# Optimization experiments

Hardware: AMD Instinct MI355X
Metric: run time of the kernel (lower is better)

The kernel has to match this reference:

```python
import jax, jax.numpy as jnp
import numpy as np

NUM_HEADS = 8  # matches init_kwargs num_heads
LN_EPS = 1e-5  # torch.nn.LayerNorm default


def setup_inputs() -> dict:
    key = jax.random.key(0)
    ks = jax.random.split(key, 12)
    E, B, H, S = 16384, 16, 256, 32
    edge_features = jax.random.normal(ks[0], (E, H), jnp.float32)
    edge_coords = jax.random.normal(ks[1], (E, 3), jnp.float32)
    # sorted, equal-size segments (all graphs non-empty)
    batch = jnp.repeat(jnp.arange(B, dtype=jnp.int32), E // B)
    s_h = 1.0 / np.sqrt(H)
    s_sh = 1.0 / np.sqrt(S * H)
    seed_vectors = jax.random.normal(ks[2], (S, H), jnp.float32)
    # weights stored [in, out] (transposed vs torch nn.Linear)
    Wq = jax.random.normal(ks[3], (H, H), jnp.float32) * s_h
    Wk = jax.random.normal(ks[4], (H, H), jnp.float32) * s_h
    Wv = jax.random.normal(ks[5], (H, H), jnp.float32) * s_h
    Wo = jax.random.normal(ks[6], (H, H), jnp.float32) * s_h
    bo = jnp.zeros((H,), jnp.float32)
    ln_g = jnp.ones((H,), jnp.float32)
    ln_b = jnp.zeros((H,), jnp.float32)
    W1 = jax.random.normal(ks[7], (S * H, H), jnp.float32) * s_sh
    b1 = jnp.zeros((H,), jnp.float32)
    W2 = jax.random.normal(ks[8], (H, H), jnp.float32) * s_h
    b2 = jnp.zeros((H,), jnp.float32)
    return dict(edge_features=edge_features, edge_coords=edge_coords, batch=batch,
                seed_vectors=seed_vectors, Wq=Wq, Wk=Wk, Wv=Wv, Wo=Wo, bo=bo,
                ln_g=ln_g, ln_b=ln_b, W1=W1, b1=b1, W2=W2, b2=b2, num_graphs=B)


def reference(edge_features, edge_coords, batch, seed_vectors, Wq, Wk, Wv, Wo, bo,
              ln_g, ln_b, W1, b1, W2, b2, num_graphs):
    S, H = seed_vectors.shape
    nh = NUM_HEADS
    hd = H // nh
    q = (seed_vectors @ Wq).reshape(S, nh, hd)          # shared across graphs
    k = (edge_features @ Wk).reshape(-1, nh, hd)        # [E, nh, hd]
    v = (edge_features @ Wv).reshape(-1, nh, hd)
    scores = jnp.einsum('shd,ehd->esh', q, k) / np.sqrt(hd).astype(np.float32)
    # segment softmax over edges within each graph
    m = jax.lax.stop_gradient(jax.ops.segment_max(scores, batch, num_segments=num_graphs))
    num = jnp.exp(scores - m[batch])
    den = jax.ops.segment_sum(num, batch, num_segments=num_graphs)
    w = num / den[batch]                                # [E, S, nh]
    att = jax.ops.segment_sum(jnp.einsum('esh,ehd->eshd', w, v), batch,
                              num_segments=num_graphs)  # [B, S, nh, hd]
    att = att.reshape(num_graphs, S, H)                 # concat heads (head-major)
    y = seed_vectors[None, :, :] + att @ Wo + bo        # residual + out_proj
    mu = jnp.mean(y, axis=-1, keepdims=True)
    var = jnp.mean((y - mu) ** 2, axis=-1, keepdims=True)
    y = (y - mu) / jnp.sqrt(var + LN_EPS) * ln_g + ln_b
    flat = y.reshape(num_graphs, S * H)
    h1 = jax.nn.silu(flat @ W1 + b1)
    return h1 @ W2 + b2                                 # [B, H]
```

## Files before the change

### kernel.cpp

```cpp
#include <hip/hip_runtime.h>
#include <math.h>
#include <stdint.h>

#define E_EDGES 16384
#define H_DIM   256
#define S_SEEDS 32
#define NHEADS  8
#define HDIM    32
#define BGRAPHS 16
#define EPG     1024
#define NCHUNK  256
#define CPG     16
#define RSQRT_HD 0.17677669529663687f

typedef __attribute__((ext_vector_type(8))) short bf16x8;
typedef __attribute__((ext_vector_type(4))) float f32x4;

__device__ inline unsigned short f2bf(float x) {
    unsigned u = __float_as_uint(x);
    u += 0x7fff + ((u >> 16) & 1);
    return (unsigned short)(u >> 16);
}
__device__ inline float bf2f(unsigned int h) {
    return __uint_as_float((h & 0xffffu) << 16);
}
__device__ inline unsigned pack2(float a, float b) {
    return (unsigned)f2bf(a) | ((unsigned)f2bf(b) << 16);
}

__global__ __launch_bounds__(256) void k_wc(const float* __restrict__ Wv,
                                            const float* __restrict__ Wk,
                                            const float* __restrict__ Wq,
                                            const float* __restrict__ seed,
                                            unsigned short* __restrict__ WcT) {
    int j = blockIdx.x;
    int i = threadIdx.x;
    float val;
    if (j < H_DIM) {
        val = Wv[i * H_DIM + j];
    } else {
        int c = j - H_DIM;
        int h = c >> 5, s = c & 31;
        __shared__ float qp[8][33];
        __shared__ float qrow[HDIM];
        int d = i & 31, g = i >> 5;
        const float* wq = &Wq[(g * 32) * H_DIM + h * HDIM + d];
        const float* sd = &seed[s * H_DIM + g * 32];
        float p = 0.f;
        #pragma unroll
        for (int ii = 0; ii < 32; ++ii)
            p = fmaf(sd[ii], wq[(size_t)ii * H_DIM], p);
        qp[g][d] = p;
        __syncthreads();
        if (i < HDIM) {
            float qv = 0.f;
            #pragma unroll
            for (int g2 = 0; g2 < 8; ++g2) qv += qp[g2][i];
            qrow[i] = qv;
        }
        __syncthreads();
        const float* wk = &Wk[i * H_DIM + h * HDIM];
        float acc = 0.f;
        #pragma unroll
        for (int dd = 0; dd < HDIM; dd += 4) {
            float4 w = *(const float4*)&wk[dd];
            float4 qq = *(const float4*)&qrow[dd];
            acc = fmaf(w.x, qq.x, acc); acc = fmaf(w.y, qq.y, acc);
            acc = fmaf(w.z, qq.z, acc); acc = fmaf(w.w, qq.w, acc);
        }
        val = acc * RSQRT_HD;
    }
    WcT[j * H_DIM + i] = f2bf(val);
}

struct SMattn {
    unsigned short As[64][264];
    unsigned short Vt[256][72];
    unsigned short Pt[256][72];
};

__global__ __launch_bounds__(512) void k_attn(const float* __restrict__ A,
                                              const unsigned short* __restrict__ WcT,
                                              float* __restrict__ outc,
                                              float* __restrict__ mg,
                                              float* __restrict__ sg) {
    __shared__ SMattn sm;
    int tid = threadIdx.x;
    int chunk = blockIdx.x;
    int e0 = chunk * 64;
    int w = tid >> 6, lane = tid & 63;
    int lr = lane & 15, kg = lane >> 4;

    {
        int r = tid >> 3, cg8 = tid & 7;
        const float* ap = &A[(size_t)(e0 + r) * H_DIM + cg8 * 32];
        #pragma unroll
        for (int i = 0; i < 4; ++i) {
            float4 x = *(const float4*)&ap[i * 8];
            float4 y = *(const float4*)&ap[i * 8 + 4];
            uint4 o;
            o.x = pack2(x.x, x.y); o.y = pack2(x.z, x.w);
            o.z = pack2(y.x, y.y); o.w = pack2(y.z, y.w);
            *(uint4*)&sm.As[r][cg8 * 32 + i * 8] = o;
        }
    }
    __syncthreads();

    const unsigned short* brow = &WcT[(size_t)(w * 64 + lr) * H_DIM + kg * 8];
    uint4 bfr[2][4];
    #pragma unroll
    for (int ni = 0; ni < 4; ++ni) {
        bfr[0][ni] = *(const uint4*)(brow + (size_t)ni * 16 * H_DIM);
        bfr[1][ni] = *(const uint4*)(brow + (size_t)ni * 16 * H_DIM + 32);
    }
    f32x4 acc[4][4] = {};
    #pragma unroll
    for (int k = 0; k < 8; ++k) {
        bf16x8 af[4], bv[4];
        #pragma unroll
        for (int mi = 0; mi < 4; ++mi)
            af[mi] = *(const bf16x8*)&sm.As[mi * 16 + lr][k * 32 + kg * 8];
        #pragma unroll
        for (int ni = 0; ni < 4; ++ni)
            bv[ni] = *(const bf16x8*)&bfr[k & 1][ni];
        if (k < 6) {
            #pragma unroll
            for (int ni = 0; ni < 4; ++ni)
                bfr[k & 1][ni] = *(const uint4*)(brow + (size_t)ni * 16 * H_DIM + (k + 2) * 32);
        }
        #pragma unroll
        for (int mi = 0; mi < 4; ++mi)
            #pragma unroll
            for (int ni = 0; ni < 4; ++ni)
                acc[mi][ni] = __builtin_amdgcn_mfma_f32_16x16x32_bf16(
                    af[mi], bv[ni], acc[mi][ni], 0, 0, 0);
    }

    if (w < 4) {
        #pragma unroll
        for (int mi = 0; mi < 4; ++mi)
            #pragma unroll
            for (int ni = 0; ni < 4; ++ni)
                #pragma unroll
                for (int r = 0; r < 4; ++r)
                    sm.Vt[w * 64 + ni * 16 + lr][mi * 16 + kg * 4 + r] =
                        f2bf(acc[mi][ni][r]);
    } else {
        int wn = (w - 4) * 64;
        #pragma unroll
        for (int ni = 0; ni < 4; ++ni) {
            float m = -1e30f;
            #pragma unroll
            for (int mi = 0; mi < 4; ++mi)
                #pragma unroll
                for (int r = 0; r < 4; ++r) m = fmaxf(m, acc[mi][ni][r]);
            m = fmaxf(m, __shfl_xor(m, 16, 64));
            m = fmaxf(m, __shfl_xor(m, 32, 64));
            float sv = 0.f;
            #pragma unroll
            for (int mi = 0; mi < 4; ++mi)
                #pragma unroll
                for (int r = 0; r < 4; ++r) {
                    float e_ = __expf(acc[mi][ni][r] - m);
                    unsigned short eb = f2bf(e_);
                    sm.Pt[wn + ni * 16 + lr][mi * 16 + kg * 4 + r] = eb;
                    sv += bf2f(eb);
                }
            sv += __shfl_xor(sv, 16, 64);
            sv += __shfl_xor(sv, 32, 64);
            if (kg == 0) {
                mg[(size_t)chunk * H_DIM + wn + ni * 16 + lr] = m;
                sg[(size_t)chunk * H_DIM + wn + ni * 16 + lr] = sv;
            }
        }
    }
    __syncthreads();

    f32x4 acc2[2][2] = {};
    #pragma unroll
    for (int ms = 0; ms < 2; ++ms)
        #pragma unroll
        for (int nd = 0; nd < 2; ++nd)
            #pragma unroll
            for (int kk = 0; kk < 2; ++kk) {
                bf16x8 pa = *(const bf16x8*)&sm.Pt[w * 32 + ms * 16 + lr][kk * 32 + kg * 8];
                bf16x8 vb = *(const bf16x8*)&sm.Vt[w * 32 + nd * 16 + lr][kk * 32 + kg * 8];
                acc2[ms][nd] = __builtin_amdgcn_mfma_f32_16x16x32_bf16(
                    pa, vb, acc2[ms][nd], 0, 0, 0);
            }
    #pragma unroll
    for (int ms = 0; ms < 2; ++ms)
        #pragma unroll
        for (int nd = 0; nd < 2; ++nd)
            #pragma unroll
            for (int r = 0; r < 4; ++r) {
                int s_ = ms * 16 + kg * 4 + r;
                int c_ = w * 32 + nd * 16 + lr;
                outc[((size_t)chunk * 32 + s_) * H_DIM + c_] = acc2[ms][nd][r];
            }
}

__device__ inline float block_sum256(float v, float* red4) {
    for (int o = 32; o > 0; o >>= 1) v += __shfl_xor(v, o, 64);
    int wid = threadIdx.x >> 6;
    if ((threadIdx.x & 63) == 0) red4[wid] = v;
    __syncthreads();
    float r = red4[0] + red4[1] + red4[2] + red4[3];
    __syncthreads();
    return r;
}

__global__ __launch_bounds__(256) void k_proj_ln(const float* __restrict__ outc,
                                                 const float* __restrict__ mg,
                                                 const float* __restrict__ sg,
                                                 const float* __restrict__ seed,
                                                 const float* __restrict__ Wo,
                                                 const float* __restrict__ bo,
                                                 const float* __restrict__ ln_g,
                                                 const float* __restrict__ ln_b,
                                                 float* __restrict__ Y) {
    int bs = blockIdx.x;
    int b = bs >> 5, s = bs & 31;
    int c = threadIdx.x;
    __shared__ float mjv[CPG][8], sgv[CPG][8], sscale[CPG][8];
    __shared__ float arow[H_DIM];
    __shared__ float red4[4];
    if (c < 128) {
        int j = c >> 3, h = c & 7;
        int sc = h * 32 + s;
        mjv[j][h] = mg[(size_t)(b * CPG + j) * H_DIM + sc];
        sgv[j][h] = sg[(size_t)(b * CPG + j) * H_DIM + sc];
    }
    __syncthreads();
    if (c < 8) {
        int h = c;
        float M = -1e30f;
        #pragma unroll
        for (int j = 0; j < CPG; ++j) M = fmaxf(M, mjv[j][h]);
        float Den = 0.f;
        #pragma unroll
        for (int j = 0; j < CPG; ++j) Den += sgv[j][h] * __expf(mjv[j][h] - M);
        float inv = 1.f / Den;
        #pragma unroll
        for (int j = 0; j < CPG; ++j) sscale[j][h] = __expf(mjv[j][h] - M) * inv;
    }
    __syncthreads();
    {
        int h = c >> 5;
        float a = 0.f;
        #pragma unroll
        for (int j = 0; j < CPG; ++j)
            a = fmaf(outc[((size_t)(b * CPG + j) * 32 + s) * H_DIM + c],
                     sscale[j][h], a);
        arow[c] = a;
    }
    __syncthreads();
    float y = bo[c] + seed[s * H_DIM + c];
    #pragma unroll 4
    for (int i = 0; i < H_DIM; ++i)
        y = fmaf(arow[i], Wo[(size_t)i * H_DIM + c], y);
    float mu = block_sum256(y, red4) * (1.f / 256.f);
    float d = y - mu;
    float var = block_sum256(d * d, red4) * (1.f / 256.f);
    Y[(size_t)bs * H_DIM + c] = d * rsqrtf(var + 1e-5f) * ln_g[c] + ln_b[c];
}

__global__ __launch_bounds__(256) void k_mlp1(const float* __restrict__ Y,
                                              const float* __restrict__ W1,
                                              float* __restrict__ part) {
    int k = blockIdx.x;
    int c = threadIdx.x;
    int s_idx = k >> 4, io = (k & 15) * 16;
    __shared__ float yl[16][17];
    {
        int b = c >> 4, ii = c & 15;
        yl[b][ii] = Y[(size_t)(b * 32 + s_idx) * H_DIM + io + ii];
    }
    __syncthreads();
    float w[16];
    #pragma unroll
    for (int ii = 0; ii < 16; ++ii)
        w[ii] = W1[(size_t)(k * 16 + ii) * H_DIM + c];
    float acc[16];
    #pragma unroll
    for (int b = 0; b < 16; ++b) acc[b] = 0.f;
    #pragma unroll
    for (int ii = 0; ii < 16; ++ii)
        #pragma unroll
        for (int b = 0; b < 16; ++b)
            acc[b] = fmaf(yl[b][ii], w[ii], acc[b]);
    #pragma unroll
    for (int b = 0; b < 16; ++b)
        part[((size_t)b * 512 + k) * H_DIM + c] = acc[b];
}

__global__ __launch_bounds__(1024) void k_mlp2(const float* __restrict__ part,
                                               const float* __restrict__ b1,
                                               const float* __restrict__ W2,
                                               const float* __restrict__ b2,
                                               float* __restrict__ out) {
    int b = blockIdx.x;
    int t = threadIdx.x;
    int c = t & 255, g = t >> 8;
    __shared__ float red[4][H_DIM];
    __shared__ float hrow[H_DIM];
    float sacc = 0.f;
    const float* pb = &part[((size_t)b * 512 + g * 128) * H_DIM + c];
    #pragma unroll 8
    for (int ch = 0; ch < 128; ++ch) sacc += pb[(size_t)ch * H_DIM];
    red[g][c] = sacc;
    __syncthreads();
    if (g == 0) {
        float s = red[0][c] + red[1][c] + red[2][c] + red[3][c] + b1[c];
        hrow[c] = s / (1.f + __expf(-s));
    }
    __syncthreads();
    float wacc = 0.f;
    #pragma unroll 4
    for (int j = g * 64; j < g * 64 + 64; ++j)
        wacc = fmaf(hrow[j], W2[(size_t)j * H_DIM + c], wacc);
    red[g][c] = wacc;
    __syncthreads();
    if (g == 0)
        out[(size_t)b * H_DIM + c] = red[0][c] + red[1][c] + red[2][c] + red[3][c] + b2[c];
}

extern "C" void kernel_launch(void* const* d_in, const int* in_sizes, int n_in,
                              void* d_out, int out_size, void* d_ws, size_t ws_size,
                              hipStream_t stream) {
    const float* edge_features = (const float*)d_in[0];
    const float* seed = (const float*)d_in[3];
    const float* Wq   = (const float*)d_in[4];
    const float* Wk   = (const float*)d_in[5];
    const float* Wv   = (const float*)d_in[6];
    const float* Wo   = (const float*)d_in[7];
    const float* bo   = (const float*)d_in[8];
    const float* ln_g = (const float*)d_in[9];
    const float* ln_b = (const float*)d_in[10];
    const float* W1   = (const float*)d_in[11];
    const float* b1   = (const float*)d_in[12];
    const float* W2   = (const float*)d_in[13];
    const float* b2   = (const float*)d_in[14];
    float* out = (float*)d_out;

    float* ws = (float*)d_ws;
    unsigned short* WcT = (unsigned short*)ws;
    float* outc = ws + 65536;
    float* mg   = outc + 2097152;
    float* sg   = mg + 65536;
    float* Y    = sg + 65536;
    float* part = Y + 131072;

    k_wc      <<<512, 256, 0, stream>>>(Wv, Wk, Wq, seed, WcT);
    k_attn    <<<NCHUNK, 512, 0, stream>>>(edge_features, WcT, outc, mg, sg);
    k_proj_ln <<<512, 256, 0, stream>>>(outc, mg, sg, seed, Wo, bo, ln_g, ln_b, Y);
    k_mlp1    <<<512, 256, 0, stream>>>(Y, W1, part);
    k_mlp2    <<<BGRAPHS, 1024, 0, stream>>>(part, b1, W2, b2, out);
}
```

Baseline: 150.4 us.

## Fuse first MLP layer into projection/LayerNorm kernel and shrink partial sums

Merges the W1 matvec into the per-(graph, seed) projection+LayerNorm kernel, so each block multiplies its normalized row against the W1 slice for its seed. This removes one kernel launch and the intermediate Y buffer, and reduces the partial sums reduced by the last kernel from 512 to 32 per graph. The cost is that each W1 slice is now read by 16 blocks (one per graph) instead of once with register reuse across graphs, which greatly increases W1 read traffic.

```diff
diff --git a/kernel.cpp b/kernel.cpp
--- a/kernel.cpp
+++ b/kernel.cpp
@@ -210,20 +210,22 @@
     return r;
 }
 
-__global__ __launch_bounds__(256) void k_proj_ln(const float* __restrict__ outc,
-                                                 const float* __restrict__ mg,
-                                                 const float* __restrict__ sg,
-                                                 const float* __restrict__ seed,
-                                                 const float* __restrict__ Wo,
-                                                 const float* __restrict__ bo,
-                                                 const float* __restrict__ ln_g,
-                                                 const float* __restrict__ ln_b,
-                                                 float* __restrict__ Y) {
+__global__ __launch_bounds__(256) void k_tail(const float* __restrict__ outc,
+                                              const float* __restrict__ mg,
+                                              const float* __restrict__ sg,
+                                              const float* __restrict__ seed,
+                                              const float* __restrict__ Wo,
+                                              const float* __restrict__ bo,
+                                              const float* __restrict__ ln_g,
+                                              const float* __restrict__ ln_b,
+                                              const float* __restrict__ W1,
+                                              float* __restrict__ part) {
     int bs = blockIdx.x;
     int b = bs >> 5, s = bs & 31;
     int c = threadIdx.x;
     __shared__ float mjv[CPG][8], sgv[CPG][8], sscale[CPG][8];
     __shared__ float arow[H_DIM];
+    __shared__ float ynorm[H_DIM];
     __shared__ float red4[4];
     if (c < 128) {
         int j = c >> 3, h = c & 7;
@@ -262,36 +264,16 @@
     float mu = block_sum256(y, red4) * (1.f / 256.f);
     float d = y - mu;
     float var = block_sum256(d * d, red4) * (1.f / 256.f);
-    Y[(size_t)bs * H_DIM + c] = d * rsqrtf(var + 1e-5f) * ln_g[c] + ln_b[c];
-}
-
-__global__ __launch_bounds__(256) void k_mlp1(const float* __restrict__ Y,
-                                              const float* __restrict__ W1,
-                                              float* __restrict__ part) {
-    int k = blockIdx.x;
-    int c = threadIdx.x;
-    int s_idx = k >> 4, io = (k & 15) * 16;
-    __shared__ float yl[16][17];
+    ynorm[c] = d * rsqrtf(var + 1e-5f) * ln_g[c] + ln_b[c];
+    __syncthreads();
     {
-        int b = c >> 4, ii = c & 15;
-        yl[b][ii] = Y[(size_t)(b * 32 + s_idx) * H_DIM + io + ii];
-    }
-    __syncthreads();
-    float w[16];
-    #pragma unroll
-    for (int ii = 0; ii < 16; ++ii)
-        w[ii] = W1[(size_t)(k * 16 + ii) * H_DIM + c];
-    float acc[16];
-    #pragma unroll
-    for (int b = 0; b < 16; ++b) acc[b] = 0.f;
-    #pragma unroll
-    for (int ii = 0; ii < 16; ++ii)
-        #pragma unroll
-        for (int b = 0; b < 16; ++b)
-            acc[b] = fmaf(yl[b][ii], w[ii], acc[b]);
-    #pragma unroll
-    for (int b = 0; b < 16; ++b)
-        part[((size_t)b * 512 + k) * H_DIM + c] = acc[b];
+        const float* w1p = &W1[(size_t)(s * H_DIM) * H_DIM + c];
+        float acc = 0.f;
+        #pragma unroll 4
+        for (int i = 0; i < H_DIM; ++i)
+            acc = fmaf(ynorm[i], w1p[(size_t)i * H_DIM], acc);
+        part[((size_t)s * BGRAPHS + b) * H_DIM + c] = acc;
+    }
 }
 
 __global__ __launch_bounds__(1024) void k_mlp2(const float* __restrict__ part,
@@ -305,9 +287,9 @@
     __shared__ float red[4][H_DIM];
     __shared__ float hrow[H_DIM];
     float sacc = 0.f;
-    const float* pb = &part[((size_t)b * 512 + g * 128) * H_DIM + c];
-    #pragma unroll 8
-    for (int ch = 0; ch < 128; ++ch) sacc += pb[(size_t)ch * H_DIM];
+    #pragma unroll
+    for (int sc2 = g * 8; sc2 < g * 8 + 8; ++sc2)
+        sacc += part[((size_t)sc2 * BGRAPHS + b) * H_DIM + c];
     red[g][c] = sacc;
     __syncthreads();
     if (g == 0) {
@@ -348,12 +330,10 @@
     float* outc = ws + 65536;
     float* mg   = outc + 2097152;
     float* sg   = mg + 65536;
-    float* Y    = sg + 65536;
-    float* part = Y + 131072;
-
-    k_wc      <<<512, 256, 0, stream>>>(Wv, Wk, Wq, seed, WcT);
-    k_attn    <<<NCHUNK, 512, 0, stream>>>(edge_features, WcT, outc, mg, sg);
-    k_proj_ln <<<512, 256, 0, stream>>>(outc, mg, sg, seed, Wo, bo, ln_g, ln_b, Y);
-    k_mlp1    <<<512, 256, 0, stream>>>(Y, W1, part);
-    k_mlp2    <<<BGRAPHS, 1024, 0, stream>>>(part, b1, W2, b2, out);
-}
+    float* part = sg + 65536;
+
+    k_wc   <<<512, 256, 0, stream>>>(Wv, Wk, Wq, seed, WcT);
+    k_attn <<<NCHUNK, 512, 0, stream>>>(edge_features, WcT, outc, mg, sg);
+    k_tail <<<512, 256, 0, stream>>>(outc, mg, sg, seed, Wo, bo, ln_g, ln_b, W1, part);
+    k_mlp2 <<<BGRAPHS, 1024, 0, stream>>>(part, b1, W2, b2, out);
+}
```

Result: slower. 156.8 us (+4.2%).
